# Optimization experiments

Measured on AMD Instinct MI355X. Metric: run time of the kernel, lower is better.

## Reference

```python
import math
import jax, jax.numpy as jnp
import numpy as np

N_HEAD = 16

def setup_inputs() -> dict:
    key = jax.random.key(0)
    k1, k2, k3 = jax.random.split(key, 3)
    B, T, C = 4, 2048, 1024
    x = jax.random.normal(k1, (B, T, C), dtype=jnp.float32)
    Wqkv = jax.random.normal(k2, (C, 3 * C), dtype=jnp.float32) * (1.0 / math.sqrt(C))
    bqkv = jnp.zeros((3 * C,), dtype=jnp.float32)
    Wproj = jax.random.normal(k3, (C, C), dtype=jnp.float32) * (1.0 / math.sqrt(C))
    bproj = jnp.zeros((C,), dtype=jnp.float32)
    return {"x": x, "Wqkv": Wqkv, "bqkv": bqkv, "Wproj": Wproj, "bproj": bproj}

def reference(x, Wqkv, bqkv, Wproj, bproj):
    B, T, C = x.shape
    H = N_HEAD
    D = C // H
    # fused QKV projection
    qkv = x @ Wqkv + bqkv                      # [B,T,3C]
    qkv = qkv.reshape(B, T, 3, H, D).transpose(0, 2, 3, 1, 4)  # [B,3,H,T,D]
    q, k, v = qkv[:, 0], qkv[:, 1], qkv[:, 2]  # each [B,H,T,D]
    scale = 1.0 / math.sqrt(D)
    att = jnp.einsum('bhtd,bhsd->bhts', q, k) * scale  # [B,H,T,T]
    # causal mask: disallow s > t
    mask = jnp.triu(jnp.ones((T, T), dtype=bool), k=1)
    att = jnp.where(mask, jnp.float32(-1e9), att)
    att = jax.nn.softmax(att, axis=-1)
    y = jnp.einsum('bhts,bhsd->bhtd', att, v)  # [B,H,T,D]
    y = y.transpose(0, 2, 1, 3).reshape(B, T, C)
    y = y @ Wproj + bproj
    return y
```

## Files before the change

kernel.cpp:

```cpp
#include <hip/hip_runtime.h>
#include <hip/hip_bf16.h>

#define B_ 4
#define T_ 2048
#define C_ 1024
#define H_ 16
#define D_ 64

typedef __attribute__((ext_vector_type(8))) short short8;
typedef __attribute__((ext_vector_type(4))) float f32x4;

#define QSCALE 0.18033688011112042f

static __device__ __forceinline__ unsigned short f2bf(float f) {
  unsigned u = __float_as_uint(f);
  u += 0x7fff + ((u >> 16) & 1);
  return (unsigned short)(u >> 16);
}

static __device__ __forceinline__ unsigned cvt_pk_bf16(float lo, float hi) {
  unsigned r;
  asm("v_cvt_pk_bf16_f32 %0, %1, %2" : "=v"(r) : "v"(lo), "v"(hi));
  return r;
}

static __device__ __forceinline__ float fast_exp2(float x) {
#if __has_builtin(__builtin_amdgcn_exp2f)
  return __builtin_amdgcn_exp2f(x);
#else
  return exp2f(x);
#endif
}

#define GL2LDS16(g, l)                                              \
  __builtin_amdgcn_global_load_lds(                                 \
      (const __attribute__((address_space(1))) void*)(g),           \
      (__attribute__((address_space(3))) void*)(l), 16, 0, 0)

__global__ __launch_bounds__(256) void prepass(
    const float* __restrict__ x, const float* __restrict__ Wq,
    const float* __restrict__ Wp, ushort* __restrict__ xb,
    ushort* __restrict__ Wqt, ushort* __restrict__ Wpt) {
  __shared__ ushort tile[32][33];
  const int bid = blockIdx.x;
  if (bid < 8192) {
    const size_t i = ((size_t)bid * 256 + threadIdx.x) * 4;
    float4 vv = *(const float4*)(x + i);
    ushort4 o = {f2bf(vv.x), f2bf(vv.y), f2bf(vv.z), f2bf(vv.w)};
    *(ushort4*)(xb + i) = o;
    return;
  }
  const float* in;
  ushort* out;
  int N, tix;
  if (bid < 8192 + 3072) {
    in = Wq; out = Wqt; N = 3 * C_; tix = bid - 8192;
  } else {
    in = Wp; out = Wpt; N = C_; tix = bid - 11264;
  }
  const int nT = N >> 5;
  const int k0 = (tix / nT) << 5, n0 = (tix % nT) << 5;
  const int r = threadIdx.x >> 3;
  const int c4 = (threadIdx.x & 7) << 2;
  float4 v = *(const float4*)(in + (size_t)(k0 + r) * N + n0 + c4);
  tile[c4 + 0][r] = f2bf(v.x);
  tile[c4 + 1][r] = f2bf(v.y);
  tile[c4 + 2][r] = f2bf(v.z);
  tile[c4 + 3][r] = f2bf(v.w);
  __syncthreads();
  ushort4 o = {tile[r][c4], tile[r][c4 + 1], tile[r][c4 + 2], tile[r][c4 + 3]};
  *(ushort4*)(out + (size_t)(n0 + r) * C_ + k0 + c4) = o;
}

static __device__ __forceinline__ void swz_src64(int wave, int lane, int p,
                                                 int& row, int& offU) {
  const int flat = p * 4096 + wave * 1024 + lane * 16;
  row = flat >> 7;
  const int pos = (flat & 127) >> 4;
  const int x = pos ^ (row & 7);
  offU = x * 8;
}
static __device__ __forceinline__ int swz_frag64(int r, int quad, int ko) {
  return r * 128 + (((quad | (ko << 2)) ^ (r & 7)) << 4);
}

__global__ __launch_bounds__(256) void gemm_qkv_mfma(
    const ushort* __restrict__ A, const ushort* __restrict__ Bt,
    const float* __restrict__ bias, ushort* __restrict__ q,
    ushort* __restrict__ k, ushort* __restrict__ v) {
  __shared__ __align__(16) ushort As[128 * 64];
  __shared__ __align__(16) ushort Bs[128 * 64];
  const int tid = threadIdx.x;
  const int wave = tid >> 6, lane = tid & 63;
  const int c = lane & 15, quad = lane >> 4;
  const int wm = wave & 1, wn = wave >> 1;
  const int m0 = blockIdx.y << 7;
  const int n0 = blockIdx.x << 7;

  int sRow[4], sOff[4];
#pragma unroll
  for (int p = 0; p < 4; ++p) swz_src64(wave, lane, p, sRow[p], sOff[p]);
  int fOffA[2][4], fOffB[2][4];
#pragma unroll
  for (int ko = 0; ko < 2; ++ko) {
#pragma unroll
    for (int i = 0; i < 4; ++i)
      fOffA[ko][i] = swz_frag64(wm * 64 + i * 16 + c, quad, ko);
#pragma unroll
    for (int j = 0; j < 4; ++j)
      fOffB[ko][j] = swz_frag64(wn * 64 + j * 16 + c, quad, ko);
  }

  f32x4 acc[4][4];
#pragma unroll
  for (int i = 0; i < 4; ++i)
#pragma unroll
    for (int j = 0; j < 4; ++j) acc[i][j] = (f32x4){0.f, 0.f, 0.f, 0.f};

  for (int k0 = 0; k0 < C_; k0 += 64) {
    __syncthreads();
#pragma unroll
    for (int p = 0; p < 4; ++p) {
      GL2LDS16(A + (size_t)(m0 + sRow[p]) * C_ + k0 + sOff[p],
               (char*)As + p * 4096 + wave * 1024);
      GL2LDS16(Bt + (size_t)(n0 + sRow[p]) * C_ + k0 + sOff[p],
               (char*)Bs + p * 4096 + wave * 1024);
    }
    __syncthreads();
#pragma unroll
    for (int ko = 0; ko < 2; ++ko) {
      short8 af[4], bf[4];
#pragma unroll
      for (int i = 0; i < 4; ++i)
        af[i] = *(const short8*)((const char*)As + fOffA[ko][i]);
#pragma unroll
      for (int j = 0; j < 4; ++j)
        bf[j] = *(const short8*)((const char*)Bs + fOffB[ko][j]);
#pragma unroll
      for (int i = 0; i < 4; ++i)
#pragma unroll
        for (int j = 0; j < 4; ++j)
          acc[i][j] = __builtin_amdgcn_mfma_f32_16x16x32_bf16(af[i], bf[j],
                                                              acc[i][j], 0, 0, 0);
    }
  }

  const int s = n0 >> 10;
  if (s == 2) {
#pragma unroll
    for (int j = 0; j < 4; ++j) {
      const int n = n0 + wn * 64 + j * 16 + c;
      const int h = (n >> 6) & 15, d = n & 63;
      const float bval = bias[n];
#pragma unroll
      for (int i = 0; i < 4; ++i) {
        const int m = m0 + wm * 64 + i * 16 + quad * 4;
        const int b = m >> 11, t = m & 2047;
        ushort4 pk = {f2bf(acc[i][j][0] + bval), f2bf(acc[i][j][1] + bval),
                      f2bf(acc[i][j][2] + bval), f2bf(acc[i][j][3] + bval)};
        *(ushort4*)(v + (((size_t)((b << 4) + h) << 6) + d) * T_ + t) = pk;
      }
    }
  } else {
    ushort* outp = (s == 0) ? q : k;
    const float sc = (s == 0) ? QSCALE : 1.0f;
#pragma unroll
    for (int j = 0; j < 4; ++j) {
      const int n = n0 + wn * 64 + j * 16 + c;
      const int h = (n >> 6) & 15, d = n & 63;
      const float bval = bias[n];
#pragma unroll
      for (int i = 0; i < 4; ++i) {
#pragma unroll
        for (int r = 0; r < 4; ++r) {
          const int m = m0 + wm * 64 + i * 16 + quad * 4 + r;
          const int b = m >> 11, t = m & 2047;
          outp[(((size_t)((b << 4) + h) << 11) + t) * 64 + d] =
              f2bf((acc[i][j][r] + bval) * sc);
        }
      }
    }
  }
}

__global__ __launch_bounds__(256) void gemm_proj_mfma(
    const ushort* __restrict__ A, const ushort* __restrict__ Bt,
    const float* __restrict__ bias, float* __restrict__ out) {
  __shared__ __align__(16) ushort As[128 * 64];
  __shared__ __align__(16) ushort Bs[128 * 64];
  const int tid = threadIdx.x;
  const int wave = tid >> 6, lane = tid & 63;
  const int c = lane & 15, quad = lane >> 4;
  const int wm = wave & 1, wn = wave >> 1;
  const int m0 = blockIdx.y << 7;
  const int n0 = blockIdx.x << 7;

  int sRow[4], sOff[4];
#pragma unroll
  for (int p = 0; p < 4; ++p) swz_src64(wave, lane, p, sRow[p], sOff[p]);
  int fOffA[2][4], fOffB[2][4];
#pragma unroll
  for (int ko = 0; ko < 2; ++ko) {
#pragma unroll
    for (int i = 0; i < 4; ++i)
      fOffA[ko][i] = swz_frag64(wm * 64 + i * 16 + c, quad, ko);
#pragma unroll
    for (int j = 0; j < 4; ++j)
      fOffB[ko][j] = swz_frag64(wn * 64 + j * 16 + c, quad, ko);
  }

  f32x4 acc[4][4];
#pragma unroll
  for (int i = 0; i < 4; ++i)
#pragma unroll
    for (int j = 0; j < 4; ++j) acc[i][j] = (f32x4){0.f, 0.f, 0.f, 0.f};

  for (int k0 = 0; k0 < C_; k0 += 64) {
    __syncthreads();
#pragma unroll
    for (int p = 0; p < 4; ++p) {
      GL2LDS16(A + (size_t)(m0 + sRow[p]) * C_ + k0 + sOff[p],
               (char*)As + p * 4096 + wave * 1024);
      GL2LDS16(Bt + (size_t)(n0 + sRow[p]) * C_ + k0 + sOff[p],
               (char*)Bs + p * 4096 + wave * 1024);
    }
    __syncthreads();
#pragma unroll
    for (int ko = 0; ko < 2; ++ko) {
      short8 af[4], bf[4];
#pragma unroll
      for (int i = 0; i < 4; ++i)
        af[i] = *(const short8*)((const char*)As + fOffA[ko][i]);
#pragma unroll
      for (int j = 0; j < 4; ++j)
        bf[j] = *(const short8*)((const char*)Bs + fOffB[ko][j]);
#pragma unroll
      for (int i = 0; i < 4; ++i)
#pragma unroll
        for (int j = 0; j < 4; ++j)
          acc[i][j] = __builtin_amdgcn_mfma_f32_16x16x32_bf16(af[i], bf[j],
                                                              acc[i][j], 0, 0, 0);
    }
  }

#pragma unroll
  for (int j = 0; j < 4; ++j) {
    const int n = n0 + wn * 64 + j * 16 + c;
    const float bval = bias[n];
#pragma unroll
    for (int i = 0; i < 4; ++i) {
#pragma unroll
      for (int r = 0; r < 4; ++r) {
        const int m = m0 + wm * 64 + i * 16 + quad * 4 + r;
        out[(size_t)m * C_ + n] = acc[i][j][r] + bval;
      }
    }
  }
}

__global__ __launch_bounds__(256) void attn(const ushort* __restrict__ q,
                                            const ushort* __restrict__ k,
                                            const ushort* __restrict__ v,
                                            ushort* __restrict__ y2) {
  const int qt = 15 - (int)(blockIdx.x >> 6);
  const int bh = blockIdx.x & 63;
  const int t0 = qt << 7;
  const int w = threadIdx.x >> 6;
  const int lane = threadIdx.x & 63;
  const int c = lane & 15;
  const int quad = lane >> 4;

  const ushort* qp = q + (size_t)bh * T_ * D_;
  const ushort* kp = k + (size_t)bh * T_ * D_;
  const ushort* vp = v + (size_t)bh * D_ * T_;

  __shared__ __align__(16) ushort Ks[64][72];
  __shared__ __align__(16) ushort Vs[64][72];
  __shared__ __align__(16) ushort Ps[4][32][72];

  short8 qf[2][2];
#pragma unroll
  for (int g = 0; g < 2; ++g) {
    const ushort* qrow = qp + (size_t)(t0 + 32 * w + 16 * g + c) * D_;
    qf[g][0] = *(const short8*)(qrow + quad * 8);
    qf[g][1] = *(const short8*)(qrow + 32 + quad * 8);
  }

  const int srow = threadIdx.x >> 2;
  const int soff = (threadIdx.x & 3) << 4;

  uint4 ka, kb, va, vb;
  {
    const ushort* ks = kp + (size_t)srow * D_ + soff;
    const ushort* vs = vp + (size_t)srow * T_ + soff;
    ka = *(const uint4*)(ks);
    kb = *(const uint4*)(ks + 8);
    va = *(const uint4*)(vs);
    vb = *(const uint4*)(vs + 8);
  }

  f32x4 o[2][4];
  float l_i[2] = {0.f, 0.f};
#pragma unroll
  for (int g = 0; g < 2; ++g)
#pragma unroll
    for (int dt = 0; dt < 4; ++dt) o[g][dt] = (f32x4){0.f, 0.f, 0.f, 0.f};

  const int nb = 2 * qt + 2;
  for (int ib = 0; ib < nb; ++ib) {
    const int s0 = ib << 6;
    __syncthreads();
    *(uint4*)(&Ks[srow][soff]) = ka;
    *(uint4*)(&Ks[srow][soff + 8]) = kb;
    *(uint4*)(&Vs[srow][soff]) = va;
    *(uint4*)(&Vs[srow][soff + 8]) = vb;
    __syncthreads();

    if (ib + 1 < nb) {
      const int s1 = (ib + 1) << 6;
      const ushort* ks = kp + (size_t)(s1 + srow) * D_ + soff;
      const ushort* vs = vp + (size_t)srow * T_ + s1 + soff;
      ka = *(const uint4*)(ks);
      kb = *(const uint4*)(ks + 8);
      va = *(const uint4*)(vs);
      vb = *(const uint4*)(vs + 8);
    }

    f32x4 st[2][4];
    __builtin_amdgcn_s_setprio(1);
#pragma unroll
    for (int kt = 0; kt < 4; ++kt) {
      short8 af0 = *(const short8*)(&Ks[kt * 16 + c][quad * 8]);
      short8 af1 = *(const short8*)(&Ks[kt * 16 + c][32 + quad * 8]);
#pragma unroll
      for (int g = 0; g < 2; ++g) {
        f32x4 a = (f32x4){0.f, 0.f, 0.f, 0.f};
        a = __builtin_amdgcn_mfma_f32_16x16x32_bf16(af0, qf[g][0], a, 0, 0, 0);
        a = __builtin_amdgcn_mfma_f32_16x16x32_bf16(af1, qf[g][1], a, 0, 0, 0);
        st[g][kt] = a;
      }
    }
    __builtin_amdgcn_s_setprio(0);

#pragma unroll
    for (int g = 0; g < 2; ++g) {
      const int qbase = t0 + 32 * w + 16 * g;
      if (s0 + 63 > qbase) {
#pragma unroll
        for (int kt = 0; kt < 4; ++kt)
#pragma unroll
          for (int r = 0; r < 4; ++r)
            if (s0 + kt * 16 + 4 * quad + r > qbase + c) st[g][kt][r] = -1e30f;
      }
      float lacc = 0.f;
#pragma unroll
      for (int kt = 0; kt < 4; ++kt) {
        float p0 = fast_exp2(st[g][kt][0]);
        float p1 = fast_exp2(st[g][kt][1]);
        float p2 = fast_exp2(st[g][kt][2]);
        float p3 = fast_exp2(st[g][kt][3]);
        lacc += (p0 + p1) + (p2 + p3);
        uint2 pw = {cvt_pk_bf16(p0, p1), cvt_pk_bf16(p2, p3)};
        *(uint2*)(&Ps[w][g * 16 + c][kt * 16 + 4 * quad]) = pw;
      }
      l_i[g] += lacc;
    }

    short8 pf[2][2];
#pragma unroll
    for (int g = 0; g < 2; ++g) {
      pf[g][0] = *(const short8*)(&Ps[w][g * 16 + c][quad * 8]);
      pf[g][1] = *(const short8*)(&Ps[w][g * 16 + c][32 + quad * 8]);
    }
    __builtin_amdgcn_s_setprio(1);
#pragma unroll
    for (int dt = 0; dt < 4; ++dt) {
      short8 vf0 = *(const short8*)(&Vs[dt * 16 + c][quad * 8]);
      short8 vf1 = *(const short8*)(&Vs[dt * 16 + c][32 + quad * 8]);
#pragma unroll
      for (int g = 0; g < 2; ++g) {
        o[g][dt] =
            __builtin_amdgcn_mfma_f32_16x16x32_bf16(vf0, pf[g][0], o[g][dt], 0, 0, 0);
        o[g][dt] =
            __builtin_amdgcn_mfma_f32_16x16x32_bf16(vf1, pf[g][1], o[g][dt], 0, 0, 0);
      }
    }
    __builtin_amdgcn_s_setprio(0);
  }

  float linv[2];
#pragma unroll
  for (int g = 0; g < 2; ++g) {
    float ls = l_i[g];
    ls += __shfl_xor(ls, 16);
    ls += __shfl_xor(ls, 32);
    linv[g] = 1.0f / ls;
  }

  const int b = bh >> 4, h = bh & 15;
#pragma unroll
  for (int g = 0; g < 2; ++g) {
    const int row = t0 + 32 * w + 16 * g + c;
    ushort* dst = y2 + (size_t)(b * T_ + row) * C_ + h * 64;
#pragma unroll
    for (int dt = 0; dt < 4; ++dt) {
      uint2 ov = {cvt_pk_bf16(o[g][dt][0] * linv[g], o[g][dt][1] * linv[g]),
                  cvt_pk_bf16(o[g][dt][2] * linv[g], o[g][dt][3] * linv[g])};
      *(uint2*)(dst + dt * 16 + 4 * quad) = ov;
    }
  }
}

extern "C" void kernel_launch(void* const* d_in, const int* in_sizes, int n_in,
                              void* d_out, int out_size, void* d_ws,
                              size_t ws_size, hipStream_t stream) {
  const float* x = (const float*)d_in[0];
  const float* Wqkv = (const float*)d_in[1];
  const float* bqkv = (const float*)d_in[2];
  const float* Wproj = (const float*)d_in[3];
  const float* bproj = (const float*)d_in[4];
  float* out = (float*)d_out;

  const size_t per = (size_t)B_ * H_ * T_ * D_;
  ushort* q = (ushort*)d_ws;
  ushort* k = q + per;
  ushort* v = k + per;
  ushort* y2 = v + per;
  ushort* xb = y2 + per;
  ushort* Wqkvt = xb + per;
  ushort* Wprojt = Wqkvt + 3 * C_ * C_;

  prepass<<<dim3(12288), 256, 0, stream>>>(x, Wqkv, Wproj, xb, Wqkvt, Wprojt);
  gemm_qkv_mfma<<<dim3(24, 64), 256, 0, stream>>>(xb, Wqkvt, bqkv, q, k, v);
  attn<<<dim3(1024), 256, 0, stream>>>(q, k, v, y2);
  gemm_proj_mfma<<<dim3(8, 64), 256, 0, stream>>>(y2, Wprojt, bproj, out);
}
```

Measured before the change: 255.5 us.

## Pair causal attention query tiles per block and remap GEMM block order for XCDs

Each attention block now handles two query tiles, pi and 15-pi, so every block does the same amount of causal work. The pair shares one K/V staging pass, and the grid is halved to 512 blocks. The QKV and projection GEMMs remap block IDs so that consecutive tiles land on the same XCD, which is meant to improve L2 reuse of the A and B panels. In exchange, the attention kernel holds two sets of accumulators, which raises register pressure, and it launches fewer, longer blocks.

Result: slower. 274.1 us (+7.3%).

```diff
diff --git a/kernel.cpp b/kernel.cpp
--- a/kernel.cpp
+++ b/kernel.cpp
@@ -94,8 +94,10 @@
   const int wave = tid >> 6, lane = tid & 63;
   const int c = lane & 15, quad = lane >> 4;
   const int wm = wave & 1, wn = wave >> 1;
-  const int m0 = blockIdx.y << 7;
-  const int n0 = blockIdx.x << 7;
+  const int bid0 = blockIdx.y * 24 + blockIdx.x;
+  const int bid = (bid0 & 7) * 192 + (bid0 >> 3);
+  const int m0 = (bid / 24) << 7;
+  const int n0 = (bid % 24) << 7;
 
   int sRow[4], sOff[4];
 #pragma unroll
@@ -192,8 +194,10 @@
   const int wave = tid >> 6, lane = tid & 63;
   const int c = lane & 15, quad = lane >> 4;
   const int wm = wave & 1, wn = wave >> 1;
-  const int m0 = blockIdx.y << 7;
-  const int n0 = blockIdx.x << 7;
+  const int bid0 = blockIdx.y * 8 + blockIdx.x;
+  const int bid = (bid0 & 7) * 64 + (bid0 >> 3);
+  const int m0 = (bid >> 3) << 7;
+  const int n0 = (bid & 7) << 7;
 
   int sRow[4], sOff[4];
 #pragma unroll
@@ -262,9 +266,10 @@
                                             const ushort* __restrict__ k,
                                             const ushort* __restrict__ v,
                                             ushort* __restrict__ y2) {
-  const int qt = 15 - (int)(blockIdx.x >> 6);
+  const int pi = blockIdx.x >> 6;
   const int bh = blockIdx.x & 63;
-  const int t0 = qt << 7;
+  const int qtA = pi, qtB = 15 - pi;
+  const int t0A = qtA << 7, t0B = qtB << 7;
   const int w = threadIdx.x >> 6;
   const int lane = threadIdx.x & 63;
   const int c = lane & 15;
@@ -278,12 +283,15 @@
   __shared__ __align__(16) ushort Vs[64][72];
   __shared__ __align__(16) ushort Ps[4][32][72];
 
-  short8 qf[2][2];
+  short8 qfA[2][2], qfB[2][2];
 #pragma unroll
   for (int g = 0; g < 2; ++g) {
-    const ushort* qrow = qp + (size_t)(t0 + 32 * w + 16 * g + c) * D_;
-    qf[g][0] = *(const short8*)(qrow + quad * 8);
-    qf[g][1] = *(const short8*)(qrow + 32 + quad * 8);
+    const ushort* qa = qp + (size_t)(t0A + 32 * w + 16 * g + c) * D_;
+    const ushort* qb = qp + (size_t)(t0B + 32 * w + 16 * g + c) * D_;
+    qfA[g][0] = *(const short8*)(qa + quad * 8);
+    qfA[g][1] = *(const short8*)(qa + 32 + quad * 8);
+    qfB[g][0] = *(const short8*)(qb + quad * 8);
+    qfB[g][1] = *(const short8*)(qb + 32 + quad * 8);
   }
 
   const int srow = threadIdx.x >> 2;
@@ -299,16 +307,69 @@
     vb = *(const uint4*)(vs + 8);
   }
 
-  f32x4 o[2][4];
-  float l_i[2] = {0.f, 0.f};
+  f32x4 oA[2][4], oB[2][4];
+  float lA[2] = {0.f, 0.f}, lB[2] = {0.f, 0.f};
 #pragma unroll
   for (int g = 0; g < 2; ++g)
 #pragma unroll
-    for (int dt = 0; dt < 4; ++dt) o[g][dt] = (f32x4){0.f, 0.f, 0.f, 0.f};
-
-  const int nb = 2 * qt + 2;
-  for (int ib = 0; ib < nb; ++ib) {
+    for (int dt = 0; dt < 4; ++dt) {
+      oA[g][dt] = (f32x4){0.f, 0.f, 0.f, 0.f};
+      oB[g][dt] = (f32x4){0.f, 0.f, 0.f, 0.f};
+    }
+
+  const int nbA = 2 * qtA + 2;
+  const int nbB = 2 * qtB + 2;
+
+#define QK_HALF(qf, st)                                                        \
+  do {                                                                         \
+    __builtin_amdgcn_s_setprio(1);                                             \
+    _Pragma("unroll") for (int kt = 0; kt < 4; ++kt) {                         \
+      short8 af0 = *(const short8*)(&Ks[kt * 16 + c][quad * 8]);               \
+      short8 af1 = *(const short8*)(&Ks[kt * 16 + c][32 + quad * 8]);          \
+      _Pragma("unroll") for (int g = 0; g < 2; ++g) {                          \
+        f32x4 a = (f32x4){0.f, 0.f, 0.f, 0.f};                                 \
+        a = __builtin_amdgcn_mfma_f32_16x16x32_bf16(af0, qf[g][0], a, 0, 0, 0);\
+        a = __builtin_amdgcn_mfma_f32_16x16x32_bf16(af1, qf[g][1], a, 0, 0, 0);\
+        st[g][kt] = a;                                                         \
+      }                                                                        \
+    }                                                                          \
+    __builtin_amdgcn_s_setprio(0);                                             \
+  } while (0)
+
+#define SM_HALF(st, t0X, lX)                                                   \
+  do {                                                                         \
+    _Pragma("unroll") for (int g = 0; g < 2; ++g) {                            \
+      const int qbase = t0X + 32 * w + 16 * g;                                 \
+      if (s0 + 63 > qbase) {                                                   \
+        _Pragma("unroll") for (int kt = 0; kt < 4; ++kt)                       \
+            _Pragma("unroll") for (int r = 0; r < 4; ++r) if (                 \
+                s0 + kt * 16 + 4 * quad + r > qbase + c) st[g][kt][r] = -1e30f;\
+      }                                                                        \
+      float lacc = 0.f;                                                        \
+      _Pragma("unroll") for (int kt = 0; kt < 4; ++kt) {                       \
+        float p0 = fast_exp2(st[g][kt][0]);                                    \
+        float p1 = fast_exp2(st[g][kt][1]);                                    \
+        float p2 = fast_exp2(st[g][kt][2]);                                    \
+        float p3 = fast_exp2(st[g][kt][3]);                                    \
+        lacc += (p0 + p1) + (p2 + p3);                                         \
+        uint2 pw = {cvt_pk_bf16(p0, p1), cvt_pk_bf16(p2, p3)};                 \
+        *(uint2*)(&Ps[w][g * 16 + c][kt * 16 + 4 * quad]) = pw;                \
+      }                                                                        \
+      lX[g] += lacc;                                                           \
+    }                                                                          \
+  } while (0)
+
+#define PF_READ(pf)                                                            \
+  do {                                                                         \
+    _Pragma("unroll") for (int g = 0; g < 2; ++g) {                            \
+      pf[g][0] = *(const short8*)(&Ps[w][g * 16 + c][quad * 8]);               \
+      pf[g][1] = *(const short8*)(&Ps[w][g * 16 + c][32 + quad * 8]);          \
+    }                                                                          \
+  } while (0)
+
+  for (int ib = 0; ib < nbB; ++ib) {
     const int s0 = ib << 6;
+    const bool actA = ib < nbA;
     __syncthreads();
     *(uint4*)(&Ks[srow][soff]) = ka;
     *(uint4*)(&Ks[srow][soff + 8]) = kb;
@@ -316,7 +377,7 @@
     *(uint4*)(&Vs[srow][soff + 8]) = vb;
     __syncthreads();
 
-    if (ib + 1 < nb) {
+    if (ib + 1 < nbB) {
       const int s1 = (ib + 1) << 6;
       const ushort* ks = kp + (size_t)(s1 + srow) * D_ + soff;
       const ushort* vs = vp + (size_t)srow * T_ + s1 + soff;
@@ -327,88 +388,89 @@
     }
 
     f32x4 st[2][4];
+    QK_HALF(qfB, st);
+    SM_HALF(st, t0B, lB);
+    short8 pfB[2][2];
+    PF_READ(pfB);
+
+    short8 pfA[2][2];
+    if (actA) {
+      QK_HALF(qfA, st);
+      SM_HALF(st, t0A, lA);
+      PF_READ(pfA);
+    }
+
     __builtin_amdgcn_s_setprio(1);
-#pragma unroll
-    for (int kt = 0; kt < 4; ++kt) {
-      short8 af0 = *(const short8*)(&Ks[kt * 16 + c][quad * 8]);
-      short8 af1 = *(const short8*)(&Ks[kt * 16 + c][32 + quad * 8]);
-#pragma unroll
-      for (int g = 0; g < 2; ++g) {
-        f32x4 a = (f32x4){0.f, 0.f, 0.f, 0.f};
-        a = __builtin_amdgcn_mfma_f32_16x16x32_bf16(af0, qf[g][0], a, 0, 0, 0);
-        a = __builtin_amdgcn_mfma_f32_16x16x32_bf16(af1, qf[g][1], a, 0, 0, 0);
-        st[g][kt] = a;
+    if (actA) {
+#pragma unroll
+      for (int dt = 0; dt < 4; ++dt) {
+        short8 vf0 = *(const short8*)(&Vs[dt * 16 + c][quad * 8]);
+        short8 vf1 = *(const short8*)(&Vs[dt * 16 + c][32 + quad * 8]);
+#pragma unroll
+        for (int g = 0; g < 2; ++g) {
+          oB[g][dt] = __builtin_amdgcn_mfma_f32_16x16x32_bf16(vf0, pfB[g][0],
+                                                              oB[g][dt], 0, 0, 0);
+          oB[g][dt] = __builtin_amdgcn_mfma_f32_16x16x32_bf16(vf1, pfB[g][1],
+                                                              oB[g][dt], 0, 0, 0);
+          oA[g][dt] = __builtin_amdgcn_mfma_f32_16x16x32_bf16(vf0, pfA[g][0],
+                                                              oA[g][dt], 0, 0, 0);
+          oA[g][dt] = __builtin_amdgcn_mfma_f32_16x16x32_bf16(vf1, pfA[g][1],
+                                                              oA[g][dt], 0, 0, 0);
+        }
       }
+    } else {
+#pragma unroll
+      for (int dt = 0; dt < 4; ++dt) {
+        short8 vf0 = *(const short8*)(&Vs[dt * 16 + c][quad * 8]);
+        short8 vf1 = *(const short8*)(&Vs[dt * 16 + c][32 + quad * 8]);
+#pragma unroll
+        for (int g = 0; g < 2; ++g) {
+          oB[g][dt] = __builtin_amdgcn_mfma_f32_16x16x32_bf16(vf0, pfB[g][0],
+                                                              oB[g][dt], 0, 0, 0);
+          oB[g][dt] = __builtin_amdgcn_mfma_f32_16x16x32_bf16(vf1, pfB[g][1],
+                                                              oB[g][dt], 0, 0, 0);
+        }
+      }
     }
     __builtin_amdgcn_s_setprio(0);
-
-#pragma unroll
-    for (int g = 0; g < 2; ++g) {
-      const int qbase = t0 + 32 * w + 16 * g;
-      if (s0 + 63 > qbase) {
-#pragma unroll
-        for (int kt = 0; kt < 4; ++kt)
-#pragma unroll
-          for (int r = 0; r < 4; ++r)
-            if (s0 + kt * 16 + 4 * quad + r > qbase + c) st[g][kt][r] = -1e30f;
-      }
-      float lacc = 0.f;
-#pragma unroll
-      for (int kt = 0; kt < 4; ++kt) {
-        float p0 = fast_exp2(st[g][kt][0]);
-        float p1 = fast_exp2(st[g][kt][1]);
-        float p2 = fast_exp2(st[g][kt][2]);
-        float p3 = fast_exp2(st[g][kt][3]);
-        lacc += (p0 + p1) + (p2 + p3);
-        uint2 pw = {cvt_pk_bf16(p0, p1), cvt_pk_bf16(p2, p3)};
-        *(uint2*)(&Ps[w][g * 16 + c][kt * 16 + 4 * quad]) = pw;
-      }
-      l_i[g] += lacc;
-    }
-
-    short8 pf[2][2];
-#pragma unroll
-    for (int g = 0; g < 2; ++g) {
-      pf[g][0] = *(const short8*)(&Ps[w][g * 16 + c][quad * 8]);
-      pf[g][1] = *(const short8*)(&Ps[w][g * 16 + c][32 + quad * 8]);
-    }
-    __builtin_amdgcn_s_setprio(1);
-#pragma unroll
-    for (int dt = 0; dt < 4; ++dt) {
-      short8 vf0 = *(const short8*)(&Vs[dt * 16 + c][quad * 8]);
-      short8 vf1 = *(const short8*)(&Vs[dt * 16 + c][32 + quad * 8]);
-#pragma unroll
-      for (int g = 0; g < 2; ++g) {
-        o[g][dt] =
-            __builtin_amdgcn_mfma_f32_16x16x32_bf16(vf0, pf[g][0], o[g][dt], 0, 0, 0);
-        o[g][dt] =
-            __builtin_amdgcn_mfma_f32_16x16x32_bf16(vf1, pf[g][1], o[g][dt], 0, 0, 0);
-      }
-    }
-    __builtin_amdgcn_s_setprio(0);
-  }
-
-  float linv[2];
+  }
+
+  float linvA[2], linvB[2];
 #pragma unroll
   for (int g = 0; g < 2; ++g) {
-    float ls = l_i[g];
+    float ls = lB[g];
     ls += __shfl_xor(ls, 16);
     ls += __shfl_xor(ls, 32);
-    linv[g] = 1.0f / ls;
+    linvB[g] = 1.0f / ls;
+    float la = lA[g];
+    la += __shfl_xor(la, 16);
+    la += __shfl_xor(la, 32);
+    linvA[g] = 1.0f / la;
   }
 
   const int b = bh >> 4, h = bh & 15;
 #pragma unroll
   for (int g = 0; g < 2; ++g) {
-    const int row = t0 + 32 * w + 16 * g + c;
-    ushort* dst = y2 + (size_t)(b * T_ + row) * C_ + h * 64;
+    const int rowB = t0B + 32 * w + 16 * g + c;
+    ushort* dstB = y2 + (size_t)(b * T_ + rowB) * C_ + h * 64;
 #pragma unroll
     for (int dt = 0; dt < 4; ++dt) {
-      uint2 ov = {cvt_pk_bf16(o[g][dt][0] * linv[g], o[g][dt][1] * linv[g]),
-                  cvt_pk_bf16(o[g][dt][2] * linv[g], o[g][dt][3] * linv[g])};
-      *(uint2*)(dst + dt * 16 + 4 * quad) = ov;
-    }
-  }
+      uint2 ov = {cvt_pk_bf16(oB[g][dt][0] * linvB[g], oB[g][dt][1] * linvB[g]),
+                  cvt_pk_bf16(oB[g][dt][2] * linvB[g], oB[g][dt][3] * linvB[g])};
+      *(uint2*)(dstB + dt * 16 + 4 * quad) = ov;
+    }
+    const int rowA = t0A + 32 * w + 16 * g + c;
+    ushort* dstA = y2 + (size_t)(b * T_ + rowA) * C_ + h * 64;
+#pragma unroll
+    for (int dt = 0; dt < 4; ++dt) {
+      uint2 ov = {cvt_pk_bf16(oA[g][dt][0] * linvA[g], oA[g][dt][1] * linvA[g]),
+                  cvt_pk_bf16(oA[g][dt][2] * linvA[g], oA[g][dt][3] * linvA[g])};
+      *(uint2*)(dstA + dt * 16 + 4 * quad) = ov;
+    }
+  }
+#undef QK_HALF
+#undef SM_HALF
+#undef PF_READ
 }
 
 extern "C" void kernel_launch(void* const* d_in, const int* in_sizes, int n_in,
@@ -432,6 +494,6 @@
 
   prepass<<<dim3(12288), 256, 0, stream>>>(x, Wqkv, Wproj, xb, Wqkvt, Wprojt);
   gemm_qkv_mfma<<<dim3(24, 64), 256, 0, stream>>>(xb, Wqkvt, bqkv, q, k, v);
-  attn<<<dim3(1024), 256, 0, stream>>>(q, k, v, y2);
+  attn<<<dim3(512), 256, 0, stream>>>(q, k, v, y2);
   gemm_proj_mfma<<<dim3(8, 64), 256, 0, stream>>>(y2, Wprojt, bproj, out);
 }
```

## Fuse x fp32-to-bf16 conversion into QKV GEMM and remap block order

Applied to the files above, without the earlier changes.

The separate prepass that converted x to bf16 is removed. The QKV GEMM now loads fp32 x tiles into registers, converts them with v_cvt_pk_bf16 and stores them to LDS, prefetching the next k-tile while the MFMAs run. Both GEMMs also remap block IDs so that consecutive workgroups are spread across the grid, aiming for better L2/XCD locality. This saves a full write and re-read of the bf16 activation, but each QKV block (24 column blocks per row tile) now reads x at twice the bytes and uses more registers.

Measured after the change: 271.0 us. 6.0% more time.

```diff
diff --git a/kernel.cpp b/kernel.cpp
--- a/kernel.cpp
+++ b/kernel.cpp
@@ -38,25 +38,17 @@
       (__attribute__((address_space(3))) void*)(l), 16, 0, 0)
 
 __global__ __launch_bounds__(256) void prepass(
-    const float* __restrict__ x, const float* __restrict__ Wq,
-    const float* __restrict__ Wp, ushort* __restrict__ xb,
+    const float* __restrict__ Wq, const float* __restrict__ Wp,
     ushort* __restrict__ Wqt, ushort* __restrict__ Wpt) {
   __shared__ ushort tile[32][33];
   const int bid = blockIdx.x;
-  if (bid < 8192) {
-    const size_t i = ((size_t)bid * 256 + threadIdx.x) * 4;
-    float4 vv = *(const float4*)(x + i);
-    ushort4 o = {f2bf(vv.x), f2bf(vv.y), f2bf(vv.z), f2bf(vv.w)};
-    *(ushort4*)(xb + i) = o;
-    return;
-  }
   const float* in;
   ushort* out;
   int N, tix;
-  if (bid < 8192 + 3072) {
-    in = Wq; out = Wqt; N = 3 * C_; tix = bid - 8192;
+  if (bid < 3072) {
+    in = Wq; out = Wqt; N = 3 * C_; tix = bid;
   } else {
-    in = Wp; out = Wpt; N = C_; tix = bid - 11264;
+    in = Wp; out = Wpt; N = C_; tix = bid - 3072;
   }
   const int nT = N >> 5;
   const int k0 = (tix / nT) << 5, n0 = (tix % nT) << 5;
@@ -85,7 +77,7 @@
 }
 
 __global__ __launch_bounds__(256) void gemm_qkv_mfma(
-    const ushort* __restrict__ A, const ushort* __restrict__ Bt,
+    const float* __restrict__ X, const ushort* __restrict__ Bt,
     const float* __restrict__ bias, ushort* __restrict__ q,
     ushort* __restrict__ k, ushort* __restrict__ v) {
   __shared__ __align__(16) ushort As[128 * 64];
@@ -94,8 +86,10 @@
   const int wave = tid >> 6, lane = tid & 63;
   const int c = lane & 15, quad = lane >> 4;
   const int wm = wave & 1, wn = wave >> 1;
-  const int m0 = blockIdx.y << 7;
-  const int n0 = blockIdx.x << 7;
+  const int bid0 = blockIdx.y * 24 + blockIdx.x;
+  const int bid = (bid0 & 7) * 192 + (bid0 >> 3);
+  const int m0 = (bid / 24) << 7;
+  const int n0 = (bid % 24) << 7;
 
   int sRow[4], sOff[4];
 #pragma unroll
@@ -117,16 +111,35 @@
 #pragma unroll
     for (int j = 0; j < 4; ++j) acc[i][j] = (f32x4){0.f, 0.f, 0.f, 0.f};
 
+  float4 aR[4][2];
+#pragma unroll
+  for (int p = 0; p < 4; ++p) {
+    const float* s = X + (size_t)(m0 + sRow[p]) * C_ + sOff[p];
+    aR[p][0] = *(const float4*)(s);
+    aR[p][1] = *(const float4*)(s + 4);
+  }
+
   for (int k0 = 0; k0 < C_; k0 += 64) {
     __syncthreads();
 #pragma unroll
     for (int p = 0; p < 4; ++p) {
-      GL2LDS16(A + (size_t)(m0 + sRow[p]) * C_ + k0 + sOff[p],
-               (char*)As + p * 4096 + wave * 1024);
+      uint4 wv = {cvt_pk_bf16(aR[p][0].x, aR[p][0].y),
+                  cvt_pk_bf16(aR[p][0].z, aR[p][0].w),
+                  cvt_pk_bf16(aR[p][1].x, aR[p][1].y),
+                  cvt_pk_bf16(aR[p][1].z, aR[p][1].w)};
+      *(uint4*)((char*)As + p * 4096 + wave * 1024 + lane * 16) = wv;
       GL2LDS16(Bt + (size_t)(n0 + sRow[p]) * C_ + k0 + sOff[p],
                (char*)Bs + p * 4096 + wave * 1024);
     }
     __syncthreads();
+    if (k0 + 64 < C_) {
+#pragma unroll
+      for (int p = 0; p < 4; ++p) {
+        const float* s = X + (size_t)(m0 + sRow[p]) * C_ + k0 + 64 + sOff[p];
+        aR[p][0] = *(const float4*)(s);
+        aR[p][1] = *(const float4*)(s + 4);
+      }
+    }
 #pragma unroll
     for (int ko = 0; ko < 2; ++ko) {
       short8 af[4], bf[4];
@@ -192,8 +205,10 @@
   const int wave = tid >> 6, lane = tid & 63;
   const int c = lane & 15, quad = lane >> 4;
   const int wm = wave & 1, wn = wave >> 1;
-  const int m0 = blockIdx.y << 7;
-  const int n0 = blockIdx.x << 7;
+  const int bid0 = blockIdx.y * 8 + blockIdx.x;
+  const int bid = (bid0 & 7) * 64 + (bid0 >> 3);
+  const int m0 = (bid >> 3) << 7;
+  const int n0 = (bid & 7) << 7;
 
   int sRow[4], sOff[4];
 #pragma unroll
@@ -426,12 +441,11 @@
   ushort* k = q + per;
   ushort* v = k + per;
   ushort* y2 = v + per;
-  ushort* xb = y2 + per;
-  ushort* Wqkvt = xb + per;
+  ushort* Wqkvt = y2 + per;
   ushort* Wprojt = Wqkvt + 3 * C_ * C_;
 
-  prepass<<<dim3(12288), 256, 0, stream>>>(x, Wqkv, Wproj, xb, Wqkvt, Wprojt);
-  gemm_qkv_mfma<<<dim3(24, 64), 256, 0, stream>>>(xb, Wqkvt, bqkv, q, k, v);
+  prepass<<<dim3(4096), 256, 0, stream>>>(Wqkv, Wproj, Wqkvt, Wprojt);
+  gemm_qkv_mfma<<<dim3(24, 64), 256, 0, stream>>>(x, Wqkvt, bqkv, q, k, v);
   attn<<<dim3(1024), 256, 0, stream>>>(q, k, v, y2);
   gemm_proj_mfma<<<dim3(8, 64), 256, 0, stream>>>(y2, Wprojt, bproj, out);
 }
```
